# Kernel optimization log

Measured on AMD Instinct MI355X. Metric: run time of the kernel, lower is better.

The kernel has to match this reference:

```python
import jax, jax.numpy as jnp
import numpy as np

B, S, D = 2, 2048, 1024
H, HD = 16, 64  # num heads, head dim
EPS = 1e-12
SCALING = HD ** -0.5


def rotate_half(x):
    x1, x2 = jnp.split(x, 2, axis=-1)
    return jnp.concatenate([-x2, x1], axis=-1)


def setup_inputs() -> dict:
    key = jax.random.key(0)
    ks = jax.random.split(key, 12)
    hidden_states = jax.random.normal(ks[0], (B, S, D), dtype=jnp.float32)
    # RoPE tables (standard rotate-half convention)
    inv_freq = 1.0 / (10000.0 ** (np.arange(0, HD, 2, dtype=np.float32) / HD))
    pos = np.arange(S, dtype=np.float32)
    freqs = np.outer(pos, inv_freq)  # [S, HD/2]
    emb = np.concatenate([freqs, freqs], axis=-1)  # [S, HD]
    cos = jnp.asarray(np.cos(emb))
    sin = jnp.asarray(np.sin(emb))
    w = 0.02
    return {
        "hidden_states": hidden_states,
        "cos": cos,
        "sin": sin,
        "Wq": jax.random.normal(ks[1], (D, D), dtype=jnp.float32) * w,
        "bq": jnp.zeros((D,), dtype=jnp.float32),
        "Wk": jax.random.normal(ks[2], (D, D), dtype=jnp.float32) * w,
        "bk": jnp.zeros((D,), dtype=jnp.float32),
        "Wv": jax.random.normal(ks[3], (D, D), dtype=jnp.float32) * w,
        "bv": jnp.zeros((D,), dtype=jnp.float32),
        "Wo": jax.random.normal(ks[4], (D, D), dtype=jnp.float32) * w,
        "bo": jnp.zeros((D,), dtype=jnp.float32),
        "ln_w": jnp.ones((D,), dtype=jnp.float32),
        "ln_b": jnp.zeros((D,), dtype=jnp.float32),
    }


def reference(hidden_states, cos, sin, Wq, bq, Wk, bk, Wv, bv, Wo, bo, ln_w, ln_b):
    b, s, d = hidden_states.shape
    # QKV projections -> [b, h, s, hd]
    def proj(W, bias):
        return (hidden_states @ W.T + bias).reshape(b, s, H, HD).transpose(0, 2, 1, 3)
    q, k, v = proj(Wq, bq), proj(Wk, bk), proj(Wv, bv)
    # RoPE (cos/sin broadcast over batch and head dims)
    c = cos[None, None, :, :]
    sn = sin[None, None, :, :]
    q = q * c + rotate_half(q) * sn
    k = k * c + rotate_half(k) * sn
    # Faithful to source: query pre-scaled AND scaling applied inside attention
    q = q * SCALING
    scores = jnp.einsum("bhsd,bhtd->bhst", q, k) * SCALING
    attn = jax.nn.softmax(scores, axis=-1)
    ctx = jnp.einsum("bhst,bhtd->bhsd", attn, v)  # [b,h,s,hd]
    ctx = ctx.transpose(0, 2, 1, 3).reshape(b, s, d)
    # output dense + residual + LayerNorm
    out = ctx @ Wo.T + bo + hidden_states
    mu = jnp.mean(out, axis=-1, keepdims=True)
    var = jnp.var(out, axis=-1, keepdims=True)
    return (out - mu) / jnp.sqrt(var + EPS) * ln_w + ln_b
```

## Files before the change

kernel.cpp:

```cpp
#include <hip/hip_runtime.h>
#include <hip/hip_bf16.h>
#include <stdint.h>


typedef unsigned short ushort_t;
typedef short bf16x8 __attribute__((ext_vector_type(8)));
typedef float f32x4 __attribute__((ext_vector_type(4)));
typedef float f32x16 __attribute__((ext_vector_type(16)));
typedef unsigned short ushort8 __attribute__((ext_vector_type(8)));

#define LOG2E 1.4426950408889634f

__device__ __forceinline__ ushort_t f2b(float f) {
  uint32_t x = __builtin_bit_cast(uint32_t, f);
  return (ushort_t)((x + 0x7FFFu + ((x >> 16) & 1u)) >> 16);
}

__device__ __forceinline__ uint32_t cvt_pk_bf16(float lo, float hi) {
  uint32_t r;
  asm("v_cvt_pk_bf16_f32 %0, %1, %2" : "=v"(r) : "v"(lo), "v"(hi));
  return r;
}

__device__ __forceinline__ void permswap(uint32_t& a, uint32_t& b) {
  asm volatile("v_permlane32_swap_b32 %0, %1" : "+v"(a), "+v"(b));
}

__device__ __forceinline__ void gload16(const void* gptr, void* ldsptr) {
  __builtin_amdgcn_global_load_lds(
      (const __attribute__((address_space(1))) uint32_t*)gptr,
      (__attribute__((address_space(3))) uint32_t*)ldsptr, 16, 0, 0);
}

__global__ void cast_kernel(const float* __restrict__ src, ushort_t* __restrict__ dst, int n) {
  int i = (blockIdx.x * 256 + threadIdx.x) * 8;
  if (i >= n) return;
  const float4* s = (const float4*)(src + i);
  float4 a = s[0], b = s[1];
  ushort8 o = { f2b(a.x), f2b(a.y), f2b(a.z), f2b(a.w),
                f2b(b.x), f2b(b.y), f2b(b.z), f2b(b.w) };
  *(ushort8*)(dst + i) = o;
}

__global__ void cast4_kernel(const float* __restrict__ a, const float* __restrict__ b,
                             const float* __restrict__ c, const float* __restrict__ d2,
                             ushort_t* __restrict__ oa, ushort_t* __restrict__ ob,
                             ushort_t* __restrict__ oc, ushort_t* __restrict__ od) {
  const int which = blockIdx.x >> 9;
  const float* src = which == 0 ? a : which == 1 ? b : which == 2 ? c : d2;
  ushort_t* dst = which == 0 ? oa : which == 1 ? ob : which == 2 ? oc : od;
  int i = ((blockIdx.x & 511) * 256 + threadIdx.x) * 8;
  const float4* s = (const float4*)(src + i);
  float4 x = s[0], y = s[1];
  ushort8 o = { f2b(x.x), f2b(x.y), f2b(x.z), f2b(x.w),
                f2b(y.x), f2b(y.y), f2b(y.z), f2b(y.w) };
  *(ushort8*)(dst + i) = o;
}

__global__ __launch_bounds__(256) void gemm_qkv(
    const ushort_t* __restrict__ hid, const ushort_t* __restrict__ wq,
    const ushort_t* __restrict__ wk, const ushort_t* __restrict__ wv,
    const float* __restrict__ bq, const float* __restrict__ bk,
    const float* __restrict__ bv, const float* __restrict__ cosT,
    const float* __restrict__ sinT, ushort_t* __restrict__ qout,
    ushort_t* __restrict__ kout, ushort_t* __restrict__ vtout)
{
  constexpr int K = 1024;
  __shared__ uint4 SB[3072];
  const int which = blockIdx.z;
  const ushort_t* A;
  const ushort_t* Bm;
  const float* bias;
  int m0, n0;
  if (which == 0)      { A = hid; Bm = wq; bias = bq; m0 = blockIdx.x * 128; n0 = blockIdx.y * 128; }
  else if (which == 1) { A = hid; Bm = wk; bias = bk; m0 = blockIdx.x * 128; n0 = blockIdx.y * 128; }
  else                 { A = wv;  Bm = hid; bias = bv; m0 = blockIdx.y * 128; n0 = blockIdx.x * 128; }

  const int tid = threadIdx.x;
  const int wave = tid >> 6, lane = tid & 63;
  const int d = lane & 15, g = lane >> 4;
  const int wm = (wave >> 1) * 64, wn = (wave & 1) * 64;

  const ushort_t* ag = A + (size_t)(m0 + (tid >> 2)) * K + (tid & 3) * 8;
  const ushort_t* bg = Bm + (size_t)(n0 + (tid >> 2)) * K + (tid & 3) * 8;

  f32x4 acc[4][4] = {};

#define STAGE_Q(buf, k0)                                           \
  {                                                                \
    char* dst = (char*)SB + (buf) * 16384 + wave * 1024;           \
    gload16(ag + (k0), dst);                                       \
    gload16(ag + 64 * K + (k0), dst + 4096);                       \
    gload16(bg + (k0), dst + 8192);                                \
    gload16(bg + 64 * K + (k0), dst + 12288);                      \
  }

#define COMPUTE_Q(buf)                                                          \
  {                                                                             \
    bf16x8 af[4], bfr[4];                                                       \
    _Pragma("unroll") for (int i = 0; i < 4; ++i)                               \
        af[i] = __builtin_bit_cast(bf16x8,                                      \
            SB[(buf) * 1024 + (wm + i * 16 + d) * 4 + g]);                      \
    _Pragma("unroll") for (int j = 0; j < 4; ++j)                               \
        bfr[j] = __builtin_bit_cast(bf16x8,                                     \
            SB[(buf) * 1024 + 512 + (wn + j * 16 + d) * 4 + g]);                \
    _Pragma("unroll") for (int i = 0; i < 4; ++i)                               \
        _Pragma("unroll") for (int j = 0; j < 4; ++j)                           \
            acc[i][j] = __builtin_amdgcn_mfma_f32_16x16x32_bf16(                \
                af[i], bfr[j], acc[i][j], 0, 0, 0);                             \
  }

  STAGE_Q(0, 0);
  STAGE_Q(1, 32);
  asm volatile("s_waitcnt vmcnt(4)" ::: "memory");
  __builtin_amdgcn_s_barrier();

  int bufc = 0;
  for (int t = 0; t < 30; ++t) {
    int bufn = bufc + 2; if (bufn >= 3) bufn -= 3;
    STAGE_Q(bufn, (t + 2) * 32);
    COMPUTE_Q(bufc);
    asm volatile("s_waitcnt vmcnt(4)" ::: "memory");
    __builtin_amdgcn_s_barrier();
    bufc = (bufc == 2) ? 0 : bufc + 1;
  }
  COMPUTE_Q(bufc);
  asm volatile("s_waitcnt vmcnt(0)" ::: "memory");
  __builtin_amdgcn_s_barrier();
  bufc = (bufc == 2) ? 0 : bufc + 1;
  COMPUTE_Q(bufc);
#undef STAGE_Q
#undef COMPUTE_Q

  if (which <= 1) {
    ushort_t* O = which == 0 ? qout : kout;
    const float qscale = which == 0 ? (LOG2E / 64.0f) : 1.0f;
    const int head_base = n0 + wn;
    const int h = head_base >> 6;
#pragma unroll
    for (int i = 0; i < 4; ++i) {
#pragma unroll
      for (int r = 0; r < 4; ++r) {
        const int m = m0 + wm + i * 16 + g * 4 + r;
        const int s = m & 2047, b = m >> 11;
#pragma unroll
        for (int j = 0; j < 4; ++j) {
          const int c = j * 16 + d;
          const float v0 = acc[i][j][r] + bias[head_base + c];
          const float v1 = acc[i][j ^ 2][r] + bias[head_base + (c ^ 32)];
          const float rot = (c < 32) ? -v1 : v1;
          const float vr = (v0 * cosT[s * 64 + c] + rot * sinT[s * 64 + c]) * qscale;
          O[(size_t)(((b << 4) + h) * 2048 + s) * 64 + c] = f2b(vr);
        }
      }
    }
  } else {
    ushort_t* O = vtout;
#pragma unroll
    for (int i = 0; i < 4; ++i) {
#pragma unroll
      for (int r = 0; r < 4; ++r) {
        const int fr = m0 + wm + i * 16 + g * 4 + r;
        const float bv2 = bias[fr];
        const int h = fr >> 6, dd = fr & 63;
#pragma unroll
        for (int j = 0; j < 4; ++j) {
          const int tok = n0 + wn + j * 16 + d;
          const int b = tok >> 11, s = tok & 2047;
          O[(size_t)(((b << 4) + h) * 64 + dd) * 2048 + s] = f2b(acc[i][j][r] + bv2);
        }
      }
    }
  }
}

__global__ __launch_bounds__(256) void gemm_wo(
    const ushort_t* __restrict__ A, const ushort_t* __restrict__ B,
    const float* __restrict__ bias, const float* __restrict__ resid,
    float* __restrict__ O)
{
  constexpr int K = 1024;
  __shared__ uint4 SB[3072];
  const int tid = threadIdx.x;
  const int wave = tid >> 6, lane = tid & 63;
  const int d = lane & 15, g = lane >> 4;
  const int m0 = blockIdx.x * 128, n0 = blockIdx.y * 128;
  const int wm = (wave >> 1) * 64, wn = (wave & 1) * 64;

  const ushort_t* ag = A + (size_t)(m0 + (tid >> 2)) * K + (tid & 3) * 8;
  const ushort_t* bg = B + (size_t)(n0 + (tid >> 2)) * K + (tid & 3) * 8;

  f32x4 acc[4][4] = {};

#define STAGE_W(buf, k0)                                           \
  {                                                                \
    char* dst = (char*)SB + (buf) * 16384 + wave * 1024;           \
    gload16(ag + (k0), dst);                                       \
    gload16(ag + 64 * K + (k0), dst + 4096);                       \
    gload16(bg + (k0), dst + 8192);                                \
    gload16(bg + 64 * K + (k0), dst + 12288);                      \
  }

#define COMPUTE_W(buf)                                                          \
  {                                                                             \
    bf16x8 af[4], bfr[4];                                                       \
    _Pragma("unroll") for (int i = 0; i < 4; ++i)                               \
        af[i] = __builtin_bit_cast(bf16x8,                                      \
            SB[(buf) * 1024 + (wm + i * 16 + d) * 4 + g]);                      \
    _Pragma("unroll") for (int j = 0; j < 4; ++j)                               \
        bfr[j] = __builtin_bit_cast(bf16x8,                                     \
            SB[(buf) * 1024 + 512 + (wn + j * 16 + d) * 4 + g]);                \
    _Pragma("unroll") for (int i = 0; i < 4; ++i)                               \
        _Pragma("unroll") for (int j = 0; j < 4; ++j)                           \
            acc[i][j] = __builtin_amdgcn_mfma_f32_16x16x32_bf16(                \
                af[i], bfr[j], acc[i][j], 0, 0, 0);                             \
  }

  STAGE_W(0, 0);
  STAGE_W(1, 32);
  asm volatile("s_waitcnt vmcnt(4)" ::: "memory");
  __builtin_amdgcn_s_barrier();

  int bufc = 0;
  for (int t = 0; t < 30; ++t) {
    int bufn = bufc + 2; if (bufn >= 3) bufn -= 3;
    STAGE_W(bufn, (t + 2) * 32);
    COMPUTE_W(bufc);
    asm volatile("s_waitcnt vmcnt(4)" ::: "memory");
    __builtin_amdgcn_s_barrier();
    bufc = (bufc == 2) ? 0 : bufc + 1;
  }
  COMPUTE_W(bufc);
  asm volatile("s_waitcnt vmcnt(0)" ::: "memory");
  __builtin_amdgcn_s_barrier();
  bufc = (bufc == 2) ? 0 : bufc + 1;
  COMPUTE_W(bufc);
#undef STAGE_W
#undef COMPUTE_W

#pragma unroll
  for (int i = 0; i < 4; ++i)
#pragma unroll
    for (int r = 0; r < 4; ++r) {
      const int m = m0 + wm + i * 16 + g * 4 + r;
#pragma unroll
      for (int j = 0; j < 4; ++j) {
        const int n = n0 + wn + j * 16 + d;
        O[(size_t)m * 1024 + n] = acc[i][j][r] + bias[n] + resid[(size_t)m * 1024 + n];
      }
    }
}

__global__ __launch_bounds__(256, 2) void attn_kernel(
    const ushort_t* __restrict__ Q, const ushort_t* __restrict__ Kb,
    const ushort_t* __restrict__ VT, ushort_t* __restrict__ ctx)
{
  __shared__ uint4 KV[2048];
  const int orig = blockIdx.x;
  const int wgid = (orig & 7) * 64 + (orig >> 3);
  const int bh = wgid >> 4;
  const int q0 = (wgid & 15) * 128;
  const int tid = threadIdx.x, wave = tid >> 6, lane = tid & 63;
  const int ql = lane & 31, h2 = lane >> 5;
  const int qrow = q0 + wave * 32 + ql;

  bf16x8 qf[4];
  {
    const ushort_t* qp = Q + ((size_t)bh * 2048 + qrow) * 64 + h2 * 8;
#pragma unroll
    for (int s = 0; s < 4; ++s)
      qf[s] = __builtin_bit_cast(bf16x8, *(const uint4*)(qp + 16 * s));
  }

  const int st_row = tid >> 3, st_c8 = tid & 7;
  const ushort_t* kgp = Kb + (size_t)(bh * 2048 + st_row) * 64 + st_c8 * 8;
  const ushort_t* vgp = VT + (size_t)(bh * 64 + st_row) * 2048 + st_c8 * 8;
  const int sidx0 = st_row * 8 + (st_c8 ^ (st_row & 7));
  const int sidx1 = (st_row + 32) * 8 + (st_c8 ^ (st_row & 7));

  uint4 kr0 = *(const uint4*)(kgp);
  uint4 kr1 = *(const uint4*)(kgp + 32 * 64);
  uint4 vr0 = *(const uint4*)(vgp);
  uint4 vr1 = *(const uint4*)(vgp + 32 * 2048);
  KV[sidx0] = kr0; KV[sidx1] = kr1;
  KV[512 + sidx0] = vr0; KV[512 + sidx1] = vr1;
  __syncthreads();

  float lsum = 0.f;
  f32x16 cacc[2] = {};

  for (int t = 0; t < 32; ++t) {
    const int cb = (t & 1) << 10;
    const int nb = ((t + 1) & 1) << 10;
    const int kvn = (t + 1) * 64;
    if (t < 31) {
      kr0 = *(const uint4*)(kgp + kvn * 64);
      kr1 = *(const uint4*)(kgp + (kvn + 32) * 64);
      vr0 = *(const uint4*)(vgp + kvn);
      vr1 = *(const uint4*)(vgp + 32 * 2048 + kvn);
    }

    f32x16 sacc[2];
#pragma unroll
    for (int jj = 0; jj < 2; ++jj) {
      f32x16 z = {};
#pragma unroll
      for (int s = 0; s < 4; ++s) {
        bf16x8 kf = __builtin_bit_cast(bf16x8,
            KV[cb + (jj * 32 + ql) * 8 + ((2 * s + h2) ^ (ql & 7))]);
        z = __builtin_amdgcn_mfma_f32_32x32x16_bf16(kf, qf[s], z, 0, 0, 0);
      }
      sacc[jj] = z;
    }

    bf16x8 pf[4];
    float ps0 = 0.f, ps1 = 0.f;
#pragma unroll
    for (int s = 0; s < 4; ++s) {
      const int jj = s >> 1;
      const int rb = (s & 1) * 8;
      float p0 = __builtin_amdgcn_exp2f(sacc[jj][rb + 0]);
      float p1 = __builtin_amdgcn_exp2f(sacc[jj][rb + 1]);
      float p2 = __builtin_amdgcn_exp2f(sacc[jj][rb + 2]);
      float p3 = __builtin_amdgcn_exp2f(sacc[jj][rb + 3]);
      float p4 = __builtin_amdgcn_exp2f(sacc[jj][rb + 4]);
      float p5 = __builtin_amdgcn_exp2f(sacc[jj][rb + 5]);
      float p6 = __builtin_amdgcn_exp2f(sacc[jj][rb + 6]);
      float p7 = __builtin_amdgcn_exp2f(sacc[jj][rb + 7]);
      ps0 += (p0 + p1) + (p2 + p3);
      ps1 += (p4 + p5) + (p6 + p7);
      uint32_t a1 = cvt_pk_bf16(p0, p1);
      uint32_t a2 = cvt_pk_bf16(p2, p3);
      uint32_t b1 = cvt_pk_bf16(p4, p5);
      uint32_t b2 = cvt_pk_bf16(p6, p7);
      permswap(a1, b1);
      permswap(a2, b2);
      uint4 u = {a1, a2, b1, b2};
      pf[s] = __builtin_bit_cast(bf16x8, u);
    }
    lsum += ps0 + ps1;

#pragma unroll
    for (int dt = 0; dt < 2; ++dt)
#pragma unroll
      for (int s = 0; s < 4; ++s) {
        bf16x8 vf = __builtin_bit_cast(bf16x8,
            KV[cb + 512 + (dt * 32 + ql) * 8 + ((2 * s + h2) ^ (ql & 7))]);
        cacc[dt] = __builtin_amdgcn_mfma_f32_32x32x16_bf16(vf, pf[s], cacc[dt], 0, 0, 0);
      }

    if (t < 31) {
      KV[nb + sidx0] = kr0; KV[nb + sidx1] = kr1;
      KV[nb + 512 + sidx0] = vr0; KV[nb + 512 + sidx1] = vr1;
    }
    __syncthreads();
  }

  lsum += __shfl_xor(lsum, 32, 64);
  const float rinv = 1.0f / lsum;
  const int b = bh >> 4, h = bh & 15;
  ushort_t* cp = ctx + ((size_t)(b * 2048 + qrow)) * 1024 + h * 64 + h2 * 4;
#pragma unroll
  for (int dt = 0; dt < 2; ++dt)
#pragma unroll
    for (int t = 0; t < 4; ++t) {
      uint2 w;
      w.x = cvt_pk_bf16(cacc[dt][4 * t + 0] * rinv, cacc[dt][4 * t + 1] * rinv);
      w.y = cvt_pk_bf16(cacc[dt][4 * t + 2] * rinv, cacc[dt][4 * t + 3] * rinv);
      *(uint2*)(cp + dt * 32 + t * 8) = w;
    }
}

__global__ __launch_bounds__(256) void ln_kernel(const float* __restrict__ x,
    const float* __restrict__ w, const float* __restrict__ b2, float* __restrict__ out)
{
  const int row = blockIdx.x, tid = threadIdx.x;
  const float4 v = ((const float4*)(x + (size_t)row * 1024))[tid];
  float s = v.x + v.y + v.z + v.w;
  float ss = v.x * v.x + v.y * v.y + v.z * v.z + v.w * v.w;
#pragma unroll
  for (int off = 32; off > 0; off >>= 1) {
    s += __shfl_down(s, off, 64);
    ss += __shfl_down(ss, off, 64);
  }
  __shared__ float red[8];
  if ((tid & 63) == 0) { red[tid >> 6] = s; red[4 + (tid >> 6)] = ss; }
  __syncthreads();
  const float S = red[0] + red[1] + red[2] + red[3];
  const float SS = red[4] + red[5] + red[6] + red[7];
  const float mu = S * (1.f / 1024.f);
  const float rstd = rsqrtf(SS * (1.f / 1024.f) - mu * mu + 1e-12f);
  const int c = tid * 4;
  float4 o;
  o.x = (v.x - mu) * rstd * w[c + 0] + b2[c + 0];
  o.y = (v.y - mu) * rstd * w[c + 1] + b2[c + 1];
  o.z = (v.z - mu) * rstd * w[c + 2] + b2[c + 2];
  o.w = (v.w - mu) * rstd * w[c + 3] + b2[c + 3];
  ((float4*)(out + (size_t)row * 1024))[tid] = o;
}

extern "C" void kernel_launch(void* const* d_in, const int* in_sizes, int n_in,
                              void* d_out, int out_size, void* d_ws, size_t ws_size,
                              hipStream_t stream) {
  const float* hidden = (const float*)d_in[0];
  const float* cosT = (const float*)d_in[1];
  const float* sinT = (const float*)d_in[2];
  const float* Wq = (const float*)d_in[3];
  const float* bq = (const float*)d_in[4];
  const float* Wk = (const float*)d_in[5];
  const float* bk = (const float*)d_in[6];
  const float* Wv = (const float*)d_in[7];
  const float* bv = (const float*)d_in[8];
  const float* Wo = (const float*)d_in[9];
  const float* bo = (const float*)d_in[10];
  const float* lnw = (const float*)d_in[11];
  const float* lnb = (const float*)d_in[12];

  char* ws = (char*)d_ws;
  const size_t MB = 1u << 20;
  ushort_t* hid_bf = (ushort_t*)(ws);
  ushort_t* wq_bf = (ushort_t*)(ws + 8 * MB);
  ushort_t* wk_bf = (ushort_t*)(ws + 10 * MB);
  ushort_t* wv_bf = (ushort_t*)(ws + 12 * MB);
  ushort_t* wo_bf = (ushort_t*)(ws + 14 * MB);
  ushort_t* q_buf = (ushort_t*)(ws + 16 * MB);
  ushort_t* k_buf = (ushort_t*)(ws + 24 * MB);
  ushort_t* vt_buf = (ushort_t*)(ws + 32 * MB);
  ushort_t* ctx_bf = (ushort_t*)(ws + 40 * MB);
  float* out_pre = (float*)(ws + 16 * MB);

  cast_kernel<<<2048, 256, 0, stream>>>(hidden, hid_bf, 4194304);
  cast4_kernel<<<2048, 256, 0, stream>>>(Wq, Wk, Wv, Wo, wq_bf, wk_bf, wv_bf, wo_bf);

  gemm_qkv<<<dim3(32, 8, 3), 256, 0, stream>>>(hid_bf, wq_bf, wk_bf, wv_bf,
                                               bq, bk, bv, cosT, sinT,
                                               q_buf, k_buf, vt_buf);
  attn_kernel<<<512, 256, 0, stream>>>(q_buf, k_buf, vt_buf, ctx_bf);
  gemm_wo<<<dim3(32, 8), 256, 0, stream>>>(ctx_bf, wo_bf, bo, hidden, out_pre);
  ln_kernel<<<4096, 256, 0, stream>>>(out_pre, lnw, lnb, (float*)d_out);
}
```

Baseline: 114.0 us.

## Split KV loop across two wave groups per block and merge partials via LDS

```diff
diff --git a/kernel.cpp b/kernel.cpp
--- a/kernel.cpp
+++ b/kernel.cpp
@@ -251,18 +251,21 @@
     }
 }
 
-__global__ __launch_bounds__(256, 2) void attn_kernel(
+__global__ __launch_bounds__(512, 2) void attn_kernel(
     const ushort_t* __restrict__ Q, const ushort_t* __restrict__ Kb,
     const ushort_t* __restrict__ VT, ushort_t* __restrict__ ctx)
 {
-  __shared__ uint4 KV[2048];
+  __shared__ uint4 KV[4096];
   const int orig = blockIdx.x;
   const int wgid = (orig & 7) * 64 + (orig >> 3);
   const int bh = wgid >> 4;
   const int q0 = (wgid & 15) * 128;
-  const int tid = threadIdx.x, wave = tid >> 6, lane = tid & 63;
+  const int tid = threadIdx.x;
+  const int wave = tid >> 6, lane = tid & 63;
+  const int grp = wave >> 2, w4 = wave & 3;
   const int ql = lane & 31, h2 = lane >> 5;
-  const int qrow = q0 + wave * 32 + ql;
+  const int qrow = q0 + w4 * 32 + ql;
+  const int GB = grp << 11;
 
   bf16x8 qf[4];
   {
@@ -272,28 +275,33 @@
       qf[s] = __builtin_bit_cast(bf16x8, *(const uint4*)(qp + 16 * s));
   }
 
-  const int st_row = tid >> 3, st_c8 = tid & 7;
+  const int stid = tid & 255;
+  const int st_row = stid >> 3, st_c8 = stid & 7;
   const ushort_t* kgp = Kb + (size_t)(bh * 2048 + st_row) * 64 + st_c8 * 8;
   const ushort_t* vgp = VT + (size_t)(bh * 64 + st_row) * 2048 + st_c8 * 8;
   const int sidx0 = st_row * 8 + (st_c8 ^ (st_row & 7));
   const int sidx1 = (st_row + 32) * 8 + (st_c8 ^ (st_row & 7));
 
-  uint4 kr0 = *(const uint4*)(kgp);
-  uint4 kr1 = *(const uint4*)(kgp + 32 * 64);
-  uint4 vr0 = *(const uint4*)(vgp);
-  uint4 vr1 = *(const uint4*)(vgp + 32 * 2048);
-  KV[sidx0] = kr0; KV[sidx1] = kr1;
-  KV[512 + sidx0] = vr0; KV[512 + sidx1] = vr1;
+  {
+    const int kv0 = grp * 64;
+    uint4 a = *(const uint4*)(kgp + kv0 * 64);
+    uint4 b = *(const uint4*)(kgp + (kv0 + 32) * 64);
+    uint4 c = *(const uint4*)(vgp + kv0);
+    uint4 e = *(const uint4*)(vgp + 32 * 2048 + kv0);
+    KV[GB + sidx0] = a; KV[GB + sidx1] = b;
+    KV[GB + 512 + sidx0] = c; KV[GB + 512 + sidx1] = e;
+  }
   __syncthreads();
 
   float lsum = 0.f;
   f32x16 cacc[2] = {};
-
-  for (int t = 0; t < 32; ++t) {
-    const int cb = (t & 1) << 10;
-    const int nb = ((t + 1) & 1) << 10;
-    const int kvn = (t + 1) * 64;
-    if (t < 31) {
+  uint4 kr0, kr1, vr0, vr1;
+
+  for (int tt = 0; tt < 16; ++tt) {
+    const int cb = GB + ((tt & 1) << 10);
+    const int nb = GB + (((tt + 1) & 1) << 10);
+    const int kvn = (2 * (tt + 1) + grp) * 64;
+    if (tt < 15) {
       kr0 = *(const uint4*)(kgp + kvn * 64);
       kr1 = *(const uint4*)(kgp + (kvn + 32) * 64);
       vr0 = *(const uint4*)(vgp + kvn);
@@ -301,6 +309,7 @@
     }
 
     f32x16 sacc[2];
+    __builtin_amdgcn_s_setprio(1);
 #pragma unroll
     for (int jj = 0; jj < 2; ++jj) {
       f32x16 z = {};
@@ -312,6 +321,7 @@
       }
       sacc[jj] = z;
     }
+    __builtin_amdgcn_s_setprio(0);
 
     bf16x8 pf[4];
     float ps0 = 0.f, ps1 = 0.f;
@@ -340,6 +350,7 @@
     }
     lsum += ps0 + ps1;
 
+    __builtin_amdgcn_s_setprio(1);
 #pragma unroll
     for (int dt = 0; dt < 2; ++dt)
 #pragma unroll
@@ -348,27 +359,48 @@
             KV[cb + 512 + (dt * 32 + ql) * 8 + ((2 * s + h2) ^ (ql & 7))]);
         cacc[dt] = __builtin_amdgcn_mfma_f32_32x32x16_bf16(vf, pf[s], cacc[dt], 0, 0, 0);
       }
-
-    if (t < 31) {
+    __builtin_amdgcn_s_setprio(0);
+
+    if (tt < 15) {
       KV[nb + sidx0] = kr0; KV[nb + sidx1] = kr1;
       KV[nb + 512 + sidx0] = vr0; KV[nb + 512 + sidx1] = vr1;
     }
     __syncthreads();
   }
 
-  lsum += __shfl_xor(lsum, 32, 64);
-  const float rinv = 1.0f / lsum;
-  const int b = bh >> 4, h = bh & 15;
-  ushort_t* cp = ctx + ((size_t)(b * 2048 + qrow)) * 1024 + h * 64 + h2 * 4;
-#pragma unroll
-  for (int dt = 0; dt < 2; ++dt)
-#pragma unroll
-    for (int t = 0; t < 4; ++t) {
-      uint2 w;
-      w.x = cvt_pk_bf16(cacc[dt][4 * t + 0] * rinv, cacc[dt][4 * t + 1] * rinv);
-      w.y = cvt_pk_bf16(cacc[dt][4 * t + 2] * rinv, cacc[dt][4 * t + 3] * rinv);
-      *(uint2*)(cp + dt * 32 + t * 8) = w;
-    }
+  float* Lf = (float*)KV;
+  const int slot = w4 * 64 + lane;
+  if (grp == 1) {
+#pragma unroll
+    for (int dt = 0; dt < 2; ++dt)
+#pragma unroll
+      for (int r = 0; r < 16; ++r)
+        Lf[slot * 32 + ((dt * 16 + r) ^ (lane & 31))] = cacc[dt][r];
+    Lf[8192 + slot] = lsum;
+  }
+  __syncthreads();
+  if (grp == 0) {
+#pragma unroll
+    for (int dt = 0; dt < 2; ++dt)
+#pragma unroll
+      for (int r = 0; r < 16; ++r)
+        cacc[dt][r] += Lf[slot * 32 + ((dt * 16 + r) ^ (lane & 31))];
+    lsum += Lf[8192 + slot];
+
+    lsum += __shfl_xor(lsum, 32, 64);
+    const float rinv = 1.0f / lsum;
+    const int b = bh >> 4, h = bh & 15;
+    ushort_t* cp = ctx + ((size_t)(b * 2048 + qrow)) * 1024 + h * 64 + h2 * 4;
+#pragma unroll
+    for (int dt = 0; dt < 2; ++dt)
+#pragma unroll
+      for (int t = 0; t < 4; ++t) {
+        uint2 w;
+        w.x = cvt_pk_bf16(cacc[dt][4 * t + 0] * rinv, cacc[dt][4 * t + 1] * rinv);
+        w.y = cvt_pk_bf16(cacc[dt][4 * t + 2] * rinv, cacc[dt][4 * t + 3] * rinv);
+        *(uint2*)(cp + dt * 32 + t * 8) = w;
+      }
+  }
 }
 
 __global__ __launch_bounds__(256) void ln_kernel(const float* __restrict__ x,
@@ -435,7 +467,7 @@
   gemm_qkv<<<dim3(32, 8, 3), 256, 0, stream>>>(hid_bf, wq_bf, wk_bf, wv_bf,
                                                bq, bk, bv, cosT, sinT,
                                                q_buf, k_buf, vt_buf);
-  attn_kernel<<<512, 256, 0, stream>>>(q_buf, k_buf, vt_buf, ctx_bf);
+  attn_kernel<<<512, 512, 0, stream>>>(q_buf, k_buf, vt_buf, ctx_bf);
   gemm_wo<<<dim3(32, 8), 256, 0, stream>>>(ctx_bf, wo_bf, bo, hidden, out_pre);
   ln_kernel<<<4096, 256, 0, stream>>>(out_pre, lnw, lnb, (float*)d_out);
 }
```

Measured after the change: 115.1 us. Within noise of the previous version (+0.9%).

## Restructure attention into 2-wave blocks with triple-buffered async K/V loads

Applied to the files above, without the earlier changes.

```diff
diff --git a/kernel.cpp b/kernel.cpp
--- a/kernel.cpp
+++ b/kernel.cpp
@@ -251,123 +251,157 @@
     }
 }
 
-__global__ __launch_bounds__(256, 2) void attn_kernel(
+__global__ __launch_bounds__(128) void attn_kernel(
     const ushort_t* __restrict__ Q, const ushort_t* __restrict__ Kb,
     const ushort_t* __restrict__ VT, ushort_t* __restrict__ ctx)
 {
-  __shared__ uint4 KV[2048];
+  __shared__ uint4 KV[3072];
   const int orig = blockIdx.x;
   const int wgid = (orig & 7) * 64 + (orig >> 3);
   const int bh = wgid >> 4;
   const int q0 = (wgid & 15) * 128;
   const int tid = threadIdx.x, wave = tid >> 6, lane = tid & 63;
   const int ql = lane & 31, h2 = lane >> 5;
-  const int qrow = q0 + wave * 32 + ql;
-
-  bf16x8 qf[4];
+  const int qrowA = q0 + wave * 64 + ql;
+
+  bf16x8 qfA[4], qfB[4];
   {
-    const ushort_t* qp = Q + ((size_t)bh * 2048 + qrow) * 64 + h2 * 8;
-#pragma unroll
-    for (int s = 0; s < 4; ++s)
-      qf[s] = __builtin_bit_cast(bf16x8, *(const uint4*)(qp + 16 * s));
-  }
-
-  const int st_row = tid >> 3, st_c8 = tid & 7;
-  const ushort_t* kgp = Kb + (size_t)(bh * 2048 + st_row) * 64 + st_c8 * 8;
-  const ushort_t* vgp = VT + (size_t)(bh * 64 + st_row) * 2048 + st_c8 * 8;
-  const int sidx0 = st_row * 8 + (st_c8 ^ (st_row & 7));
-  const int sidx1 = (st_row + 32) * 8 + (st_c8 ^ (st_row & 7));
-
-  uint4 kr0 = *(const uint4*)(kgp);
-  uint4 kr1 = *(const uint4*)(kgp + 32 * 64);
-  uint4 vr0 = *(const uint4*)(vgp);
-  uint4 vr1 = *(const uint4*)(vgp + 32 * 2048);
-  KV[sidx0] = kr0; KV[sidx1] = kr1;
-  KV[512 + sidx0] = vr0; KV[512 + sidx1] = vr1;
-  __syncthreads();
-
-  float lsum = 0.f;
-  f32x16 cacc[2] = {};
-
+    const ushort_t* qp = Q + ((size_t)bh * 2048 + qrowA) * 64 + h2 * 8;
+#pragma unroll
+    for (int s = 0; s < 4; ++s) {
+      qfA[s] = __builtin_bit_cast(bf16x8, *(const uint4*)(qp + 16 * s));
+      qfB[s] = __builtin_bit_cast(bf16x8, *(const uint4*)(qp + 32 * 64 + 16 * s));
+    }
+  }
+
+  const int srow = lane >> 3;
+  const int schunk = (lane & 7) ^ srow;
+  const ushort_t* kg = Kb + ((size_t)bh * 2048 + wave * 32 + srow) * 64 + schunk * 8;
+  const ushort_t* vg = VT + ((size_t)bh * 64 + wave * 32 + srow) * 2048 + schunk * 8;
+
+#define ATT_STAGE(buf, kv0)                                                     \
+  {                                                                             \
+    char* kb = (char*)KV + (buf) * 16384 + wave * 4096;                         \
+    char* vb = kb + 8192;                                                       \
+    _Pragma("unroll") for (int i = 0; i < 4; ++i)                               \
+        gload16(kg + ((size_t)(kv0) + i * 8) * 64, kb + i * 1024);              \
+    _Pragma("unroll") for (int i = 0; i < 4; ++i)                               \
+        gload16(vg + (kv0) + (size_t)i * 8 * 2048, vb + i * 1024);              \
+  }
+
+  float lsumA = 0.f, lsumB = 0.f;
+  f32x16 caccA[2] = {}, caccB[2] = {};
+
+  ATT_STAGE(0, 0);
+  ATT_STAGE(1, 64);
+  asm volatile("s_waitcnt vmcnt(8)" ::: "memory");
+  __builtin_amdgcn_s_barrier();
+
+  int bufc = 0;
   for (int t = 0; t < 32; ++t) {
-    const int cb = (t & 1) << 10;
-    const int nb = ((t + 1) & 1) << 10;
-    const int kvn = (t + 1) * 64;
-    if (t < 31) {
-      kr0 = *(const uint4*)(kgp + kvn * 64);
-      kr1 = *(const uint4*)(kgp + (kvn + 32) * 64);
-      vr0 = *(const uint4*)(vgp + kvn);
-      vr1 = *(const uint4*)(vgp + 32 * 2048 + kvn);
-    }
-
-    f32x16 sacc[2];
+    if (t < 30) {
+      int bufn = bufc + 2; if (bufn >= 3) bufn -= 3;
+      ATT_STAGE(bufn, (t + 2) * 64);
+    }
+    const int cb = bufc * 1024;
+
+    bf16x8 pfA[4], pfB[4];
 #pragma unroll
     for (int jj = 0; jj < 2; ++jj) {
-      f32x16 z = {};
+      f32x16 zA = {}, zB = {};
+      __builtin_amdgcn_s_setprio(1);
 #pragma unroll
       for (int s = 0; s < 4; ++s) {
         bf16x8 kf = __builtin_bit_cast(bf16x8,
             KV[cb + (jj * 32 + ql) * 8 + ((2 * s + h2) ^ (ql & 7))]);
-        z = __builtin_amdgcn_mfma_f32_32x32x16_bf16(kf, qf[s], z, 0, 0, 0);
-      }
-      sacc[jj] = z;
-    }
-
-    bf16x8 pf[4];
-    float ps0 = 0.f, ps1 = 0.f;
-#pragma unroll
-    for (int s = 0; s < 4; ++s) {
-      const int jj = s >> 1;
-      const int rb = (s & 1) * 8;
-      float p0 = __builtin_amdgcn_exp2f(sacc[jj][rb + 0]);
-      float p1 = __builtin_amdgcn_exp2f(sacc[jj][rb + 1]);
-      float p2 = __builtin_amdgcn_exp2f(sacc[jj][rb + 2]);
-      float p3 = __builtin_amdgcn_exp2f(sacc[jj][rb + 3]);
-      float p4 = __builtin_amdgcn_exp2f(sacc[jj][rb + 4]);
-      float p5 = __builtin_amdgcn_exp2f(sacc[jj][rb + 5]);
-      float p6 = __builtin_amdgcn_exp2f(sacc[jj][rb + 6]);
-      float p7 = __builtin_amdgcn_exp2f(sacc[jj][rb + 7]);
-      ps0 += (p0 + p1) + (p2 + p3);
-      ps1 += (p4 + p5) + (p6 + p7);
-      uint32_t a1 = cvt_pk_bf16(p0, p1);
-      uint32_t a2 = cvt_pk_bf16(p2, p3);
-      uint32_t b1 = cvt_pk_bf16(p4, p5);
-      uint32_t b2 = cvt_pk_bf16(p6, p7);
-      permswap(a1, b1);
-      permswap(a2, b2);
-      uint4 u = {a1, a2, b1, b2};
-      pf[s] = __builtin_bit_cast(bf16x8, u);
-    }
-    lsum += ps0 + ps1;
-
+        zA = __builtin_amdgcn_mfma_f32_32x32x16_bf16(kf, qfA[s], zA, 0, 0, 0);
+        zB = __builtin_amdgcn_mfma_f32_32x32x16_bf16(kf, qfB[s], zB, 0, 0, 0);
+      }
+      __builtin_amdgcn_s_setprio(0);
+#pragma unroll
+      for (int half = 0; half < 2; ++half) {
+        const int rb = half * 8;
+        {
+          float p0 = __builtin_amdgcn_exp2f(zA[rb + 0]);
+          float p1 = __builtin_amdgcn_exp2f(zA[rb + 1]);
+          float p2 = __builtin_amdgcn_exp2f(zA[rb + 2]);
+          float p3 = __builtin_amdgcn_exp2f(zA[rb + 3]);
+          float p4 = __builtin_amdgcn_exp2f(zA[rb + 4]);
+          float p5 = __builtin_amdgcn_exp2f(zA[rb + 5]);
+          float p6 = __builtin_amdgcn_exp2f(zA[rb + 6]);
+          float p7 = __builtin_amdgcn_exp2f(zA[rb + 7]);
+          lsumA += ((p0 + p1) + (p2 + p3)) + ((p4 + p5) + (p6 + p7));
+          uint32_t a1 = cvt_pk_bf16(p0, p1);
+          uint32_t a2 = cvt_pk_bf16(p2, p3);
+          uint32_t b1 = cvt_pk_bf16(p4, p5);
+          uint32_t b2 = cvt_pk_bf16(p6, p7);
+          permswap(a1, b1);
+          permswap(a2, b2);
+          uint4 u = {a1, a2, b1, b2};
+          pfA[jj * 2 + half] = __builtin_bit_cast(bf16x8, u);
+        }
+        {
+          float p0 = __builtin_amdgcn_exp2f(zB[rb + 0]);
+          float p1 = __builtin_amdgcn_exp2f(zB[rb + 1]);
+          float p2 = __builtin_amdgcn_exp2f(zB[rb + 2]);
+          float p3 = __builtin_amdgcn_exp2f(zB[rb + 3]);
+          float p4 = __builtin_amdgcn_exp2f(zB[rb + 4]);
+          float p5 = __builtin_amdgcn_exp2f(zB[rb + 5]);
+          float p6 = __builtin_amdgcn_exp2f(zB[rb + 6]);
+          float p7 = __builtin_amdgcn_exp2f(zB[rb + 7]);
+          lsumB += ((p0 + p1) + (p2 + p3)) + ((p4 + p5) + (p6 + p7));
+          uint32_t a1 = cvt_pk_bf16(p0, p1);
+          uint32_t a2 = cvt_pk_bf16(p2, p3);
+          uint32_t b1 = cvt_pk_bf16(p4, p5);
+          uint32_t b2 = cvt_pk_bf16(p6, p7);
+          permswap(a1, b1);
+          permswap(a2, b2);
+          uint4 u = {a1, a2, b1, b2};
+          pfB[jj * 2 + half] = __builtin_bit_cast(bf16x8, u);
+        }
+      }
+    }
+
+    __builtin_amdgcn_s_setprio(1);
 #pragma unroll
     for (int dt = 0; dt < 2; ++dt)
 #pragma unroll
       for (int s = 0; s < 4; ++s) {
         bf16x8 vf = __builtin_bit_cast(bf16x8,
             KV[cb + 512 + (dt * 32 + ql) * 8 + ((2 * s + h2) ^ (ql & 7))]);
-        cacc[dt] = __builtin_amdgcn_mfma_f32_32x32x16_bf16(vf, pf[s], cacc[dt], 0, 0, 0);
-      }
-
-    if (t < 31) {
-      KV[nb + sidx0] = kr0; KV[nb + sidx1] = kr1;
-      KV[nb + 512 + sidx0] = vr0; KV[nb + 512 + sidx1] = vr1;
-    }
-    __syncthreads();
-  }
-
-  lsum += __shfl_xor(lsum, 32, 64);
-  const float rinv = 1.0f / lsum;
+        caccA[dt] = __builtin_amdgcn_mfma_f32_32x32x16_bf16(vf, pfA[s], caccA[dt], 0, 0, 0);
+        caccB[dt] = __builtin_amdgcn_mfma_f32_32x32x16_bf16(vf, pfB[s], caccB[dt], 0, 0, 0);
+      }
+    __builtin_amdgcn_s_setprio(0);
+
+    if (t < 30) {
+      asm volatile("s_waitcnt vmcnt(8)" ::: "memory");
+    } else {
+      asm volatile("s_waitcnt vmcnt(0)" ::: "memory");
+    }
+    __builtin_amdgcn_s_barrier();
+    bufc = (bufc == 2) ? 0 : bufc + 1;
+  }
+#undef ATT_STAGE
+
+  lsumA += __shfl_xor(lsumA, 32, 64);
+  lsumB += __shfl_xor(lsumB, 32, 64);
+  const float rinvA = 1.0f / lsumA;
+  const float rinvB = 1.0f / lsumB;
   const int b = bh >> 4, h = bh & 15;
-  ushort_t* cp = ctx + ((size_t)(b * 2048 + qrow)) * 1024 + h * 64 + h2 * 4;
+  ushort_t* cpA = ctx + ((size_t)(b * 2048 + qrowA)) * 1024 + h * 64 + h2 * 4;
+  ushort_t* cpB = cpA + 32 * 1024;
 #pragma unroll
   for (int dt = 0; dt < 2; ++dt)
 #pragma unroll
     for (int t = 0; t < 4; ++t) {
       uint2 w;
-      w.x = cvt_pk_bf16(cacc[dt][4 * t + 0] * rinv, cacc[dt][4 * t + 1] * rinv);
-      w.y = cvt_pk_bf16(cacc[dt][4 * t + 2] * rinv, cacc[dt][4 * t + 3] * rinv);
-      *(uint2*)(cp + dt * 32 + t * 8) = w;
+      w.x = cvt_pk_bf16(caccA[dt][4 * t + 0] * rinvA, caccA[dt][4 * t + 1] * rinvA);
+      w.y = cvt_pk_bf16(caccA[dt][4 * t + 2] * rinvA, caccA[dt][4 * t + 3] * rinvA);
+      *(uint2*)(cpA + dt * 32 + t * 8) = w;
+      w.x = cvt_pk_bf16(caccB[dt][4 * t + 0] * rinvB, caccB[dt][4 * t + 1] * rinvB);
+      w.y = cvt_pk_bf16(caccB[dt][4 * t + 2] * rinvB, caccB[dt][4 * t + 3] * rinvB);
+      *(uint2*)(cpB + dt * 32 + t * 8) = w;
     }
 }
 
@@ -435,7 +469,7 @@
   gemm_qkv<<<dim3(32, 8, 3), 256, 0, stream>>>(hid_bf, wq_bf, wk_bf, wv_bf,
                                                bq, bk, bv, cosT, sinT,
                                                q_buf, k_buf, vt_buf);
-  attn_kernel<<<512, 256, 0, stream>>>(q_buf, k_buf, vt_buf, ctx_bf);
+  attn_kernel<<<512, 128, 0, stream>>>(q_buf, k_buf, vt_buf, ctx_bf);
   gemm_wo<<<dim3(32, 8), 256, 0, stream>>>(ctx_bf, wo_bf, bo, hidden, out_pre);
   ln_kernel<<<4096, 256, 0, stream>>>(out_pre, lnw, lnb, (float*)d_out);
 }
```

Result: slower. 145.0 us (+27.2%).

## Split each attention KV tile across two waves per query block

Applied to the files above, without the earlier changes.

```diff
diff --git a/kernel.cpp b/kernel.cpp
--- a/kernel.cpp
+++ b/kernel.cpp
@@ -251,18 +251,21 @@
     }
 }
 
-__global__ __launch_bounds__(256, 2) void attn_kernel(
+__global__ __launch_bounds__(512) void attn_kernel(
     const ushort_t* __restrict__ Q, const ushort_t* __restrict__ Kb,
     const ushort_t* __restrict__ VT, ushort_t* __restrict__ ctx)
 {
   __shared__ uint4 KV[2048];
+  __shared__ float Ls[256];
   const int orig = blockIdx.x;
   const int wgid = (orig & 7) * 64 + (orig >> 3);
   const int bh = wgid >> 4;
   const int q0 = (wgid & 15) * 128;
-  const int tid = threadIdx.x, wave = tid >> 6, lane = tid & 63;
+  const int tid = threadIdx.x;
+  const int wave = tid >> 6, lane = tid & 63;
+  const int qw = wave >> 1, half = wave & 1;
   const int ql = lane & 31, h2 = lane >> 5;
-  const int qrow = q0 + wave * 32 + ql;
+  const int qrow = q0 + qw * 32 + ql;
 
   bf16x8 qf[4];
   {
@@ -275,15 +278,12 @@
   const int st_row = tid >> 3, st_c8 = tid & 7;
   const ushort_t* kgp = Kb + (size_t)(bh * 2048 + st_row) * 64 + st_c8 * 8;
   const ushort_t* vgp = VT + (size_t)(bh * 64 + st_row) * 2048 + st_c8 * 8;
-  const int sidx0 = st_row * 8 + (st_c8 ^ (st_row & 7));
-  const int sidx1 = (st_row + 32) * 8 + (st_c8 ^ (st_row & 7));
-
-  uint4 kr0 = *(const uint4*)(kgp);
-  uint4 kr1 = *(const uint4*)(kgp + 32 * 64);
-  uint4 vr0 = *(const uint4*)(vgp);
-  uint4 vr1 = *(const uint4*)(vgp + 32 * 2048);
-  KV[sidx0] = kr0; KV[sidx1] = kr1;
-  KV[512 + sidx0] = vr0; KV[512 + sidx1] = vr1;
+  const int sidx = st_row * 8 + (st_c8 ^ (st_row & 7));
+
+  uint4 kr = *(const uint4*)(kgp);
+  uint4 vr = *(const uint4*)(vgp);
+  KV[sidx] = kr;
+  KV[512 + sidx] = vr;
   __syncthreads();
 
   float lsum = 0.f;
@@ -294,41 +294,31 @@
     const int nb = ((t + 1) & 1) << 10;
     const int kvn = (t + 1) * 64;
     if (t < 31) {
-      kr0 = *(const uint4*)(kgp + kvn * 64);
-      kr1 = *(const uint4*)(kgp + (kvn + 32) * 64);
-      vr0 = *(const uint4*)(vgp + kvn);
-      vr1 = *(const uint4*)(vgp + 32 * 2048 + kvn);
-    }
-
-    f32x16 sacc[2];
-#pragma unroll
-    for (int jj = 0; jj < 2; ++jj) {
-      f32x16 z = {};
-#pragma unroll
-      for (int s = 0; s < 4; ++s) {
-        bf16x8 kf = __builtin_bit_cast(bf16x8,
-            KV[cb + (jj * 32 + ql) * 8 + ((2 * s + h2) ^ (ql & 7))]);
-        z = __builtin_amdgcn_mfma_f32_32x32x16_bf16(kf, qf[s], z, 0, 0, 0);
-      }
-      sacc[jj] = z;
-    }
-
-    bf16x8 pf[4];
-    float ps0 = 0.f, ps1 = 0.f;
+      kr = *(const uint4*)(kgp + kvn * 64);
+      vr = *(const uint4*)(vgp + kvn);
+    }
+
+    f32x16 z = {};
 #pragma unroll
     for (int s = 0; s < 4; ++s) {
-      const int jj = s >> 1;
-      const int rb = (s & 1) * 8;
-      float p0 = __builtin_amdgcn_exp2f(sacc[jj][rb + 0]);
-      float p1 = __builtin_amdgcn_exp2f(sacc[jj][rb + 1]);
-      float p2 = __builtin_amdgcn_exp2f(sacc[jj][rb + 2]);
-      float p3 = __builtin_amdgcn_exp2f(sacc[jj][rb + 3]);
-      float p4 = __builtin_amdgcn_exp2f(sacc[jj][rb + 4]);
-      float p5 = __builtin_amdgcn_exp2f(sacc[jj][rb + 5]);
-      float p6 = __builtin_amdgcn_exp2f(sacc[jj][rb + 6]);
-      float p7 = __builtin_amdgcn_exp2f(sacc[jj][rb + 7]);
-      ps0 += (p0 + p1) + (p2 + p3);
-      ps1 += (p4 + p5) + (p6 + p7);
+      bf16x8 kf = __builtin_bit_cast(bf16x8,
+          KV[cb + (half * 32 + ql) * 8 + ((2 * s + h2) ^ (ql & 7))]);
+      z = __builtin_amdgcn_mfma_f32_32x32x16_bf16(kf, qf[s], z, 0, 0, 0);
+    }
+
+    bf16x8 pf[2];
+#pragma unroll
+    for (int s2 = 0; s2 < 2; ++s2) {
+      const int rb = s2 * 8;
+      float p0 = __builtin_amdgcn_exp2f(z[rb + 0]);
+      float p1 = __builtin_amdgcn_exp2f(z[rb + 1]);
+      float p2 = __builtin_amdgcn_exp2f(z[rb + 2]);
+      float p3 = __builtin_amdgcn_exp2f(z[rb + 3]);
+      float p4 = __builtin_amdgcn_exp2f(z[rb + 4]);
+      float p5 = __builtin_amdgcn_exp2f(z[rb + 5]);
+      float p6 = __builtin_amdgcn_exp2f(z[rb + 6]);
+      float p7 = __builtin_amdgcn_exp2f(z[rb + 7]);
+      lsum += ((p0 + p1) + (p2 + p3)) + ((p4 + p5) + (p6 + p7));
       uint32_t a1 = cvt_pk_bf16(p0, p1);
       uint32_t a2 = cvt_pk_bf16(p2, p3);
       uint32_t b1 = cvt_pk_bf16(p4, p5);
@@ -336,39 +326,59 @@
       permswap(a1, b1);
       permswap(a2, b2);
       uint4 u = {a1, a2, b1, b2};
-      pf[s] = __builtin_bit_cast(bf16x8, u);
-    }
-    lsum += ps0 + ps1;
+      pf[s2] = __builtin_bit_cast(bf16x8, u);
+    }
 
 #pragma unroll
     for (int dt = 0; dt < 2; ++dt)
 #pragma unroll
-      for (int s = 0; s < 4; ++s) {
+      for (int s2 = 0; s2 < 2; ++s2) {
+        const int s = 2 * half + s2;
         bf16x8 vf = __builtin_bit_cast(bf16x8,
             KV[cb + 512 + (dt * 32 + ql) * 8 + ((2 * s + h2) ^ (ql & 7))]);
-        cacc[dt] = __builtin_amdgcn_mfma_f32_32x32x16_bf16(vf, pf[s], cacc[dt], 0, 0, 0);
+        cacc[dt] = __builtin_amdgcn_mfma_f32_32x32x16_bf16(vf, pf[s2], cacc[dt], 0, 0, 0);
       }
 
     if (t < 31) {
-      KV[nb + sidx0] = kr0; KV[nb + sidx1] = kr1;
-      KV[nb + 512 + sidx0] = vr0; KV[nb + 512 + sidx1] = vr1;
+      KV[nb + sidx] = kr;
+      KV[nb + 512 + sidx] = vr;
     }
     __syncthreads();
   }
 
-  lsum += __shfl_xor(lsum, 32, 64);
-  const float rinv = 1.0f / lsum;
-  const int b = bh >> 4, h = bh & 15;
-  ushort_t* cp = ctx + ((size_t)(b * 2048 + qrow)) * 1024 + h * 64 + h2 * 4;
-#pragma unroll
-  for (int dt = 0; dt < 2; ++dt)
-#pragma unroll
-    for (int t = 0; t < 4; ++t) {
-      uint2 w;
-      w.x = cvt_pk_bf16(cacc[dt][4 * t + 0] * rinv, cacc[dt][4 * t + 1] * rinv);
-      w.y = cvt_pk_bf16(cacc[dt][4 * t + 2] * rinv, cacc[dt][4 * t + 3] * rinv);
-      *(uint2*)(cp + dt * 32 + t * 8) = w;
-    }
+  float* Lf = (float*)KV;
+  const int slot = qw * 64 + lane;
+  if (half == 1) {
+#pragma unroll
+    for (int dt = 0; dt < 2; ++dt)
+#pragma unroll
+      for (int r = 0; r < 16; ++r)
+        Lf[slot * 32 + ((dt * 16 + r) ^ (lane & 31))] = cacc[dt][r];
+    Ls[slot] = lsum;
+  }
+  __syncthreads();
+  if (half == 0) {
+#pragma unroll
+    for (int dt = 0; dt < 2; ++dt)
+#pragma unroll
+      for (int r = 0; r < 16; ++r)
+        cacc[dt][r] += Lf[slot * 32 + ((dt * 16 + r) ^ (lane & 31))];
+    lsum += Ls[slot];
+
+    lsum += __shfl_xor(lsum, 32, 64);
+    const float rinv = 1.0f / lsum;
+    const int b = bh >> 4, h = bh & 15;
+    ushort_t* cp = ctx + ((size_t)(b * 2048 + qrow)) * 1024 + h * 64 + h2 * 4;
+#pragma unroll
+    for (int dt = 0; dt < 2; ++dt)
+#pragma unroll
+      for (int t = 0; t < 4; ++t) {
+        uint2 w;
+        w.x = cvt_pk_bf16(cacc[dt][4 * t + 0] * rinv, cacc[dt][4 * t + 1] * rinv);
+        w.y = cvt_pk_bf16(cacc[dt][4 * t + 2] * rinv, cacc[dt][4 * t + 3] * rinv);
+        *(uint2*)(cp + dt * 32 + t * 8) = w;
+      }
+  }
 }
 
 __global__ __launch_bounds__(256) void ln_kernel(const float* __restrict__ x,
@@ -435,7 +445,7 @@
   gemm_qkv<<<dim3(32, 8, 3), 256, 0, stream>>>(hid_bf, wq_bf, wk_bf, wv_bf,
                                                bq, bk, bv, cosT, sinT,
                                                q_buf, k_buf, vt_buf);
-  attn_kernel<<<512, 256, 0, stream>>>(q_buf, k_buf, vt_buf, ctx_bf);
+  attn_kernel<<<512, 512, 0, stream>>>(q_buf, k_buf, vt_buf, ctx_bf);
   gemm_wo<<<dim3(32, 8), 256, 0, stream>>>(ctx_bf, wo_bf, bo, hidden, out_pre);
   ln_kernel<<<4096, 256, 0, stream>>>(out_pre, lnw, lnb, (float*)d_out);
 }
```

Result: no change. 111.8 us (-2.0%).
